# Optimization experiments

Hardware: AMD Instinct MI355X
Metric: run time of the kernel (lower is better)

The kernel has to match this reference:

```python
import jax, jax.numpy as jnp
import numpy as np
from jax import lax

RATE = 2
KSIZE = 3
FUSE_K = 3
PAD = 1
SCALE = 10.0
ESCAPE_NAN = 1e-4
DN = ('NCHW', 'OIHW', 'NCHW')


def _patches(x, k, s, p):
    # x: [C,H,W] -> [L, C, k, k]  (matches torch pad + unfold(2).unfold(3) + permute)
    C = x.shape[0]
    pt = lax.conv_general_dilated_patches(
        x[None], (k, k), (s, s), [(p, p), (p, p)], dimension_numbers=DN)[0]
    oh, ow = pt.shape[1], pt.shape[2]
    # feature dim ordered (c, kh, kw)
    return pt.reshape(C, k, k, oh * ow).transpose(3, 0, 1, 2)


def setup_inputs() -> dict:
    key = jax.random.key(0)
    k1, k2 = jax.random.split(key)
    f = jax.random.normal(k1, (2, 128, 128, 128), dtype=jnp.float32)
    b = jax.random.normal(k2, (2, 128, 128, 128), dtype=jnp.float32)
    mask = jnp.zeros((1, 1, 128, 128), dtype=jnp.float32)
    return {"f": f, "b": b, "mask": mask}


def reference(f, b, mask):
    B, C, H, W = f.shape
    kernel = 2 * RATE  # 4
    # raw background patches (values for conv_transpose), per sample: [L, C, 4, 4]
    raw_w = jax.vmap(lambda bi: _patches(bi, kernel, RATE, PAD))(b)
    # nearest downsample by rate (torch nearest with scale 1/2 == strided slice)
    fd = f[:, :, ::RATE, ::RATE]
    bd = b[:, :, ::RATE, ::RATE]
    md = mask[:, :, ::RATE, ::RATE]
    fh, fw = fd.shape[2], fd.shape[3]
    bh, bw = bd.shape[2], bd.shape[3]
    L = bh * bw
    # matching (key) patches: [B, L, C, 3, 3]
    w = jax.vmap(lambda bi: _patches(bi, KSIZE, 1, PAD))(bd)
    # mask patches -> mm[l] = 1 where patch mean == 0 (valid background)
    m = _patches(md[0], KSIZE, 1, PAD)           # [L, 1, 3, 3]
    mm = (jnp.mean(m, axis=(1, 2, 3)) == 0.0).astype(f.dtype)[:, None, None]  # [L,1,1]

    fuse_w = jnp.eye(FUSE_K, dtype=f.dtype).reshape(1, 1, FUSE_K, FUSE_K)

    def fuse_conv(y):
        return lax.conv_general_dilated(y, fuse_w, (1, 1), [(1, 1), (1, 1)],
                                        dimension_numbers=DN)

    def one(xi, wi, rwi):
        # xi: [C,fh,fw], wi: [L,C,3,3], rwi: [L,C,4,4]
        norm = jnp.sqrt(jnp.sum(wi * wi, axis=(1, 2, 3), keepdims=True))
        wn = wi / jnp.maximum(norm, ESCAPE_NAN)
        # correlation scores (QK^T analogue): [1, L, fh, fw]
        yi = lax.conv_general_dilated(xi[None], wn, (1, 1), [(1, 1), (1, 1)],
                                      dimension_numbers=DN)
        # diagonal fuse convs, exactly mirroring the torch view/permute sequence
        yi = yi.reshape(1, 1, fh * fw, bh * bw)
        yi = fuse_conv(yi)
        yi = yi.reshape(fh, fw, bh, bw).transpose(1, 0, 3, 2).reshape(1, 1, fh * fw, bh * bw)
        yi = fuse_conv(yi)
        yi = yi.reshape(fw, fh, bw, bh).transpose(1, 0, 3, 2)  # [fh, fw, bh, bw]
        # faithful to the torch .view (plain contiguous reshape, no transpose)
        yi = yi.reshape(bh * bw, fh, fw)
        yi = yi * mm
        yi = jax.nn.softmax(yi * SCALE, axis=0) * mm
        # conv_transpose2d(yi, rwi, stride=rate, padding=1) / 4
        wt = jnp.flip(rwi, axis=(2, 3)).transpose(1, 0, 2, 3)  # [C, L, 4, 4]
        p = kernel - 1 - PAD  # 2
        out = lax.conv_general_dilated(yi[None], wt, (1, 1), [(p, p), (p, p)],
                                       lhs_dilation=(RATE, RATE),
                                       dimension_numbers=DN) / 4.0
        return out[0]  # [C, H, W]

    y = jax.vmap(one)(fd, w, raw_w)  # [B, C, H, W]
    return y
```

## Files before the change

### kernel.cpp

```cpp
#include <hip/hip_runtime.h>

#define CC 128
#define HH 128
#define WW 128
#define DH 64
#define DW 64
#define LTOT 4096
#define K0S 384
#define K2 2048
#define SCALE_F 10.0f
#define IMG ((size_t)CC * HH * WW)

typedef __attribute__((ext_vector_type(8))) short short8;
typedef __attribute__((ext_vector_type(4))) float f32x4;

struct Prep4 { const float* src[4]; unsigned short* dst[4]; float* ssq[4]; int lo[4]; };
struct PtrN2 { const float* ssq[2]; float* invn[2]; float* mmv[2]; };
struct PtrR2 { const float* src[2]; unsigned short* dst[2]; };

__device__ __forceinline__ unsigned short f2bf(float x) {
    union { float f; unsigned u; } v; v.f = x;
    unsigned r = v.u + 0x7fffu + ((v.u >> 16) & 1u);
    return (unsigned short)(r >> 16);
}
__device__ __forceinline__ float bf2f(unsigned short b) {
    union { unsigned u; float f; } v; v.u = ((unsigned)b) << 16;
    return v.f;
}

#define GLDS16(g, l) __builtin_amdgcn_global_load_lds( \
    (const __attribute__((address_space(1))) void*)(g), \
    (__attribute__((address_space(3))) void*)(l), 16, 0, 0)

__global__ __launch_bounds__(128) void split_ds_kernel(Prep4 P) {
    __shared__ float partial[2];
    int z = blockIdx.z;
    const float* __restrict__ src = P.src[z];
    unsigned short* __restrict__ dst = P.dst[z];
    int lo_in_seg1 = P.lo[z];
    int n = blockIdx.x;
    int c = threadIdx.x;
    int ny = n >> 6, nx = n & 63;
    float v = src[((size_t)c * HH + 2 * ny) * WW + 2 * nx];
    unsigned short hi = f2bf(v);
    unsigned short lo = f2bf(v - bf2f(hi));
    unsigned short* drow = dst + (size_t)n * K0S;
    drow[c]       = hi;
    drow[128 + c] = lo_in_seg1 ? lo : hi;
    drow[256 + c] = lo_in_seg1 ? hi : lo;

    float* ssq = P.ssq[z];
    if (ssq) {
        float s2 = v * v;
#pragma unroll
        for (int o = 32; o; o >>= 1) s2 += __shfl_xor(s2, o);
        if ((threadIdx.x & 63) == 0) partial[threadIdx.x >> 6] = s2;
        __syncthreads();
        if (threadIdx.x == 0) ssq[n] = partial[0] + partial[1];
    }
}

__global__ __launch_bounds__(256) void im2col_rawt_kernel(PtrR2 P) {
    int z = blockIdx.z;
    const float* __restrict__ src = P.src[z];
    unsigned short* __restrict__ dst = P.dst[z];
    int idx = blockIdx.x * 256 + threadIdx.x;
    int p = idx & (LTOT - 1);
    int m = idx >> 12;
    int px = p & 63, py = p >> 6;
    int ke = m & 3, kd = (m >> 2) & 3, c = m >> 4;
    int yy = 2 * py - 1 + kd, xx = 2 * px - 1 + ke;
    float v = 0.f;
    if (yy >= 0 && yy < HH && xx >= 0 && xx < WW)
        v = src[((size_t)c * HH + yy) * WW + xx];
    dst[idx] = f2bf(v);
}

__global__ void norm_mm_kernel(PtrN2 P, const float* __restrict__ mask) {
    int z = blockIdx.z;
    const float* __restrict__ ssq = P.ssq[z];
    float* __restrict__ inv_norm = P.invn[z];
    float* __restrict__ mmv = P.mmv[z];
    int p = blockIdx.x * blockDim.x + threadIdx.x;
    int px = p & 63, py = p >> 6;
    float s = 0.f, ms = 0.f;
    for (int di = -1; di <= 1; ++di)
        for (int dj = -1; dj <= 1; ++dj) {
            int y = py + di, x = px + dj;
            if (y >= 0 && y < DH && x >= 0 && x < DW) {
                s += ssq[y * 64 + x];
                ms += mask[(size_t)(2 * y) * WW + 2 * x];
            }
        }
    float n = sqrtf(s);
    if (n < 1e-4f) n = 1e-4f;
    inv_norm[p] = 1.f / n;
    mmv[p] = (ms == 0.f) ? 1.f : 0.f;
}

__global__ __launch_bounds__(256) void gemm_mfma(
    const unsigned short* __restrict__ Aop, const unsigned short* __restrict__ Bop,
    float* __restrict__ C, int M, int N, int K)
{
    __shared__ short As[128 * 64];
    __shared__ short Bs[128 * 64];
    int tid = threadIdx.x;
    int wave = tid >> 6, lane = tid & 63;
    int wm = (wave >> 1) * 64;
    int wn = (wave & 1) * 64;
    int bm = blockIdx.y * 128, bn = blockIdx.x * 128;

    int rowS = wave * 32;
    int lrow8 = lane >> 3;
    int gchunk = ((lane & 7) ^ lrow8) * 8;

    f32x4 acc[4][4] = {};

    int quad = lane >> 4;
    int r16 = lane & 15;
    int pc0 = ((quad)     ^ (r16 & 7)) * 8;
    int pc1 = ((4 + quad) ^ (r16 & 7)) * 8;

    const unsigned short* ap0 = Aop + (size_t)(bm + rowS +  0 + lrow8) * K + gchunk;
    const unsigned short* ap1 = Aop + (size_t)(bm + rowS +  8 + lrow8) * K + gchunk;
    const unsigned short* ap2 = Aop + (size_t)(bm + rowS + 16 + lrow8) * K + gchunk;
    const unsigned short* ap3 = Aop + (size_t)(bm + rowS + 24 + lrow8) * K + gchunk;
    const unsigned short* bp0 = Bop + (size_t)(bn + rowS +  0 + lrow8) * K + gchunk;
    const unsigned short* bp1 = Bop + (size_t)(bn + rowS +  8 + lrow8) * K + gchunk;
    const unsigned short* bp2 = Bop + (size_t)(bn + rowS + 16 + lrow8) * K + gchunk;
    const unsigned short* bp3 = Bop + (size_t)(bn + rowS + 24 + lrow8) * K + gchunk;
    short* lA = As + rowS * 64;
    short* lB = Bs + rowS * 64;

    for (int k0 = 0; k0 < K; k0 += 64) {
        GLDS16(ap0, lA);            GLDS16(ap1, lA + 8 * 64);
        GLDS16(ap2, lA + 16 * 64);  GLDS16(ap3, lA + 24 * 64);
        GLDS16(bp0, lB);            GLDS16(bp1, lB + 8 * 64);
        GLDS16(bp2, lB + 16 * 64);  GLDS16(bp3, lB + 24 * 64);
        ap0 += 64; ap1 += 64; ap2 += 64; ap3 += 64;
        bp0 += 64; bp1 += 64; bp2 += 64; bp3 += 64;
        __syncthreads();

        short8 a0[4], b0[4], a1[4], b1[4];
#pragma unroll
        for (int i = 0; i < 4; ++i) {
            a0[i] = *(const short8*)&As[(wm + i * 16 + r16) * 64 + pc0];
            b0[i] = *(const short8*)&Bs[(wn + i * 16 + r16) * 64 + pc0];
            a1[i] = *(const short8*)&As[(wm + i * 16 + r16) * 64 + pc1];
            b1[i] = *(const short8*)&Bs[(wn + i * 16 + r16) * 64 + pc1];
        }
#pragma unroll
        for (int i = 0; i < 4; ++i)
#pragma unroll
            for (int j = 0; j < 4; ++j) {
                acc[i][j] = __builtin_amdgcn_mfma_f32_16x16x32_bf16(a0[i], b0[j], acc[i][j], 0, 0, 0);
                acc[i][j] = __builtin_amdgcn_mfma_f32_16x16x32_bf16(a1[i], b1[j], acc[i][j], 0, 0, 0);
            }
        __syncthreads();
    }

    int col = lane & 15, rq = (lane >> 4) * 4;
#pragma unroll
    for (int i = 0; i < 4; ++i) {
#pragma unroll
        for (int r = 0; r < 4; ++r) {
            int m = bm + wm + i * 16 + rq + r;
#pragma unroll
            for (int j = 0; j < 4; ++j)
                C[(size_t)m * N + bn + wn + j * 16 + col] = acc[i][j][r];
        }
    }
}

__global__ __launch_bounds__(256) void stencil_norm_kernel(
    const float* __restrict__ C, const float* __restrict__ invn,
    float* __restrict__ Sout)
{
    int blk = blockIdx.x;
    int q = ((blk & 7) << 9) | (blk >> 3);
    int t = threadIdx.x;
    int qy = q >> 6, qx = q & 63;
    int px = t & 63;
    int py0 = t >> 6;
    float acc[16] = {};
#pragma unroll
    for (int du = -1; du <= 1; ++du) {
        if (qy + du < 0 || qy + du > 63) continue;
#pragma unroll
        for (int dv = -1; dv <= 1; ++dv) {
            if (qx + dv < 0 || qx + dv > 63) continue;
            if (px + dv < 0 || px + dv > 63) continue;
            const float* row = C + (size_t)(q + 64 * du + dv) * LTOT + 64 * du + dv;
#pragma unroll
            for (int i = 0; i < 16; ++i) {
                int py = py0 + 4 * i;
                if (py + du < 0 || py + du > 63) continue;
                acc[i] += row[t + 256 * i];
            }
        }
    }
    float* orow = Sout + (size_t)q * LTOT;
#pragma unroll
    for (int i = 0; i < 16; ++i)
        orow[t + 256 * i] = acc[i] * invn[t + 256 * i];
}

__global__ __launch_bounds__(256, 4) void fused_conv_softmax_kernel(
    const float* __restrict__ S, const float* __restrict__ mmv,
    unsigned short* __restrict__ S16)
{
    __shared__ float redmax[4];
    __shared__ float redsum[4];
    int blk = blockIdx.x;
    int q = ((blk & 7) << 9) | (blk >> 3);
    int t = threadIdx.x;
    int lane = t & 63, wid = t >> 6;

    int rbase = ((q & 63) << 6) | (q >> 6);
    int rrs[3];
    bool rok[3];
#pragma unroll
    for (int j = 0; j < 3; ++j) {
        int r2 = rbase + (j - 1);
        rok[j] = (r2 >= 0) && (r2 < LTOT);
        rrs[j] = ((r2 & 63) << 6) | ((r2 >> 6) & 63);
    }

    float v[16], m[16];
#pragma unroll
    for (int i = 0; i < 16; ++i) {
        int c = t + (i << 8);
        int cbase = ((c & 63) << 6) | (c >> 6);
        float s = 0.f;
#pragma unroll
        for (int j = 0; j < 3; ++j) {
            if (!rok[j]) continue;
            int c2 = cbase + (j - 1);
            if (c2 < 0 || c2 >= LTOT) continue;
            int cc = ((c2 & 63) << 6) | (c2 >> 6);
            int rr = rrs[j];
            float tsum = 0.f;
#pragma unroll
            for (int d1 = -1; d1 <= 1; ++d1) {
                int a = rr + d1, bcol = cc + d1;
                if (a >= 0 && a < LTOT && bcol >= 0 && bcol < LTOT)
                    tsum += S[(size_t)a * LTOT + bcol];
            }
            s += tsum;
        }
        float mmx = mmv[c];
        m[i] = mmx;
        v[i] = s * mmx * SCALE_F;
    }

    float mx = v[0];
#pragma unroll
    for (int i = 1; i < 16; ++i) mx = fmaxf(mx, v[i]);
#pragma unroll
    for (int o = 32; o; o >>= 1) mx = fmaxf(mx, __shfl_xor(mx, o));
    if (lane == 0) redmax[wid] = mx;
    __syncthreads();
    float gmx = fmaxf(fmaxf(redmax[0], redmax[1]), fmaxf(redmax[2], redmax[3]));

    float s = 0.f;
#pragma unroll
    for (int i = 0; i < 16; ++i) {
        v[i] = __expf(v[i] - gmx);
        s += v[i];
    }
#pragma unroll
    for (int o = 32; o; o >>= 1) s += __shfl_xor(s, o);
    if (lane == 0) redsum[wid] = s;
    __syncthreads();
    float inv = 1.f / (redsum[0] + redsum[1] + redsum[2] + redsum[3]);

    unsigned short* orow = S16 + (size_t)q * LTOT;
#pragma unroll
    for (int i = 0; i < 16; ++i)
        orow[t + (i << 8)] = f2bf(v[i] * inv * m[i]);
}

__global__ void output_kernel(const float* __restrict__ C2t, float* __restrict__ out) {
    int idx = blockIdx.x * blockDim.x + threadIdx.x;
    int x = idx & 127;
    int y = (idx >> 7) & 127;
    int c = idx >> 14;
    int oylo = max(0, (y - 1) >> 1), oyhi = min(63, (y + 1) >> 1);
    int oxlo = max(0, (x - 1) >> 1), oxhi = min(63, (x + 1) >> 1);
    float s = 0.f;
    for (int oy = oylo; oy <= oyhi; ++oy)
        for (int ox = oxlo; ox <= oxhi; ++ox) {
            int kd = y - 2 * oy + 1;
            int ke = x - 2 * ox + 1;
            s += C2t[(size_t)(c * 16 + kd * 4 + ke) * LTOT + oy * 64 + ox];
        }
    out[idx] = s * 0.25f;
}

extern "C" void kernel_launch(void* const* d_in, const int* in_sizes, int n_in,
                              void* d_out, int out_size, void* d_ws, size_t ws_size,
                              hipStream_t stream) {
    (void)in_sizes; (void)n_in; (void)out_size; (void)ws_size;
    const float* f    = (const float*)d_in[0];
    const float* b    = (const float*)d_in[1];
    const float* mask = (const float*)d_in[2];
    float* out = (float*)d_out;

    const size_t SZ_MAT = (size_t)LTOT * LTOT * 4;
    const size_t SZ_WR  = (size_t)K2 * LTOT * 2;
    const size_t SZ_SP  = (size_t)LTOT * K0S * 2;
    const size_t SZ_V   = (size_t)LTOT * 4;

    auto pad = [](size_t n) { return (n + 255) & ~(size_t)255; };
    char* p = (char*)d_ws;
    auto take = [&](size_t n) -> void* { void* r = (void*)p; p += pad(n); return r; };

    float* Buf1 = (float*)take(SZ_MAT);
    float* Buf2 = (float*)take(SZ_MAT);
    unsigned short* W0 = (unsigned short*)take(SZ_WR);
    unsigned short* W1 = (unsigned short*)take(SZ_WR);
    unsigned short* Bsp0 = (unsigned short*)take(SZ_SP);
    unsigned short* Fsp0 = (unsigned short*)take(SZ_SP);
    unsigned short* Bsp1 = (unsigned short*)take(SZ_SP);
    unsigned short* Fsp1 = (unsigned short*)take(SZ_SP);
    float* ssq0 = (float*)take(SZ_V);  float* ssq1 = (float*)take(SZ_V);
    float* invn0 = (float*)take(SZ_V); float* invn1 = (float*)take(SZ_V);
    float* mmv0 = (float*)take(SZ_V);  float* mmv1 = (float*)take(SZ_V);

    const float* f0 = f,  *b0 = b;
    const float* f1 = f + IMG, *b1 = b + IMG;

    unsigned short* S16 = (unsigned short*)Buf1;
    float* C2t = Buf2;

    Prep4 P{{b0, f0, b1, f1}, {Bsp0, Fsp0, Bsp1, Fsp1},
            {ssq0, nullptr, ssq1, nullptr}, {1, 0, 1, 0}};
    split_ds_kernel<<<dim3(LTOT, 1, 4), 128, 0, stream>>>(P);
    PtrN2 nm{{ssq0, ssq1}, {invn0, invn1}, {mmv0, mmv1}};
    norm_mm_kernel<<<dim3(16, 1, 2), 256, 0, stream>>>(nm, mask);
    PtrR2 rw{{b0, b1}, {W0, W1}};
    im2col_rawt_kernel<<<dim3((size_t)K2 * LTOT / 256, 1, 2), 256, 0, stream>>>(rw);

    for (int bi = 0; bi < 2; ++bi) {
        const unsigned short* Fsp = bi ? Fsp1 : Fsp0;
        const unsigned short* Bsp = bi ? Bsp1 : Bsp0;
        const unsigned short* W   = bi ? W1 : W0;
        const float* invn = bi ? invn1 : invn0;
        const float* mmv  = bi ? mmv1 : mmv0;

        gemm_mfma<<<dim3(32, 32), 256, 0, stream>>>(Fsp, Bsp, Buf1, LTOT, LTOT, K0S);

        stencil_norm_kernel<<<LTOT, 256, 0, stream>>>(Buf1, invn, Buf2);

        fused_conv_softmax_kernel<<<LTOT, 256, 0, stream>>>(Buf2, mmv, S16);

        gemm_mfma<<<dim3(LTOT / 128, K2 / 128), 256, 0, stream>>>(W, S16, C2t, K2, LTOT, LTOT);

        output_kernel<<<CC * HH * WW / 256, 256, 0, stream>>>(C2t, out + (size_t)bi * IMG);
    }
}
```

Before: 598.7 us.

## Pad score matrix and vectorize stencil and fused softmax kernels

Writes the normalized score matrix into a zero-padded buffer with a row stride of 4104 floats, so the fused diagonal-conv/softmax kernel can read contiguous 16-float chunks with vector loads instead of bounds-checked scattered scalar loads. The stencil kernel now handles 16 contiguous columns per thread with vectorized loads and stores, and the softmax output is written as short8 vectors. The raw-patch im2col moves into the per-batch loop using one shared buffer, which reduces workspace. The trade-offs are unaligned vector loads, extra zeroing of the guard rows and columns, and a dependence on those zeroed pads being correct.

```diff
diff --git a/kernel.cpp b/kernel.cpp
--- a/kernel.cpp
+++ b/kernel.cpp
@@ -10,6 +10,7 @@
 #define K2 2048
 #define SCALE_F 10.0f
 #define IMG ((size_t)CC * HH * WW)
+#define PSTR 4104
 
 typedef __attribute__((ext_vector_type(8))) short short8;
 typedef __attribute__((ext_vector_type(4))) float f32x4;
@@ -26,6 +27,10 @@
 __device__ __forceinline__ float bf2f(unsigned short b) {
     union { unsigned u; float f; } v; v.u = ((unsigned)b) << 16;
     return v.f;
+}
+
+__device__ __forceinline__ f32x4 ld4u(const float* p) {
+    f32x4 r; __builtin_memcpy(&r, p, 16); return r;
 }
 
 #define GLDS16(g, l) __builtin_amdgcn_global_load_lds( \
@@ -174,39 +179,57 @@
 
 __global__ __launch_bounds__(256) void stencil_norm_kernel(
     const float* __restrict__ C, const float* __restrict__ invn,
-    float* __restrict__ Sout)
+    float* __restrict__ Sg)
 {
     int blk = blockIdx.x;
     int q = ((blk & 7) << 9) | (blk >> 3);
     int t = threadIdx.x;
     int qy = q >> 6, qx = q & 63;
-    int px = t & 63;
-    int py0 = t >> 6;
-    float acc[16] = {};
+    int chunk = t >> 2;
+    int lanebase = (t & 3) << 4;
+    int p0 = t << 4;
+
+    f32x4 acc[4];
+#pragma unroll
+    for (int g = 0; g < 4; ++g) { acc[g][0] = acc[g][1] = acc[g][2] = acc[g][3] = 0.f; }
+
 #pragma unroll
     for (int du = -1; du <= 1; ++du) {
         if (qy + du < 0 || qy + du > 63) continue;
+        if (chunk + du < 0 || chunk + du > 63) continue;
 #pragma unroll
         for (int dv = -1; dv <= 1; ++dv) {
             if (qx + dv < 0 || qx + dv > 63) continue;
-            if (px + dv < 0 || px + dv > 63) continue;
-            const float* row = C + (size_t)(q + 64 * du + dv) * LTOT + 64 * du + dv;
-#pragma unroll
-            for (int i = 0; i < 16; ++i) {
-                int py = py0 + 4 * i;
-                if (py + du < 0 || py + du > 63) continue;
-                acc[i] += row[t + 256 * i];
+            const float* rowp = C + (size_t)(q + 64 * du + dv) * LTOT + 64 * du + dv + p0;
+#pragma unroll
+            for (int g = 0; g < 4; ++g) {
+                f32x4 lv = ld4u(rowp + 4 * g);
+                if (dv == -1 && g == 0 && lanebase == 0)  lv[0] = 0.f;
+                if (dv ==  1 && g == 3 && lanebase == 48) lv[3] = 0.f;
+                acc[g] += lv;
             }
         }
     }
-    float* orow = Sout + (size_t)q * LTOT;
-#pragma unroll
-    for (int i = 0; i < 16; ++i)
-        orow[t + 256 * i] = acc[i] * invn[t + 256 * i];
-}
-
-__global__ __launch_bounds__(256, 4) void fused_conv_softmax_kernel(
-    const float* __restrict__ S, const float* __restrict__ mmv,
+    float* orow = Sg + (size_t)q * PSTR;
+#pragma unroll
+    for (int g = 0; g < 4; ++g) {
+        f32x4 iv = *(const f32x4*)(invn + p0 + 4 * g);
+        *(f32x4*)(orow + p0 + 4 * g) = acc[g] * iv;
+    }
+    if (t == 0) { orow[-4] = orow[-3] = orow[-2] = orow[-1] = 0.f; }
+    else if (t == 1) { orow[4096] = orow[4097] = orow[4098] = orow[4099] = 0.f; }
+    if (q == 0) {
+        float* gr = Sg - 4 - PSTR;
+        for (int k = t; k < PSTR; k += 256) gr[k] = 0.f;
+    }
+    if (q == 4095) {
+        float* gr = Sg - 4 + (size_t)4096 * PSTR;
+        for (int k = t; k < PSTR; k += 256) gr[k] = 0.f;
+    }
+}
+
+__global__ __launch_bounds__(256) void fused_conv_softmax_kernel(
+    const float* __restrict__ Sg, const float* __restrict__ mmv,
     unsigned short* __restrict__ S16)
 {
     __shared__ float redmax[4];
@@ -215,43 +238,50 @@
     int q = ((blk & 7) << 9) | (blk >> 3);
     int t = threadIdx.x;
     int lane = t & 63, wid = t >> 6;
+    int chunk = t >> 2;
+    int lanebase = (t & 3) << 4;
+    int c0 = t << 4;
 
     int rbase = ((q & 63) << 6) | (q >> 6);
-    int rrs[3];
-    bool rok[3];
+
+    f32x4 sacc[4];
+#pragma unroll
+    for (int g = 0; g < 4; ++g) { sacc[g][0] = sacc[g][1] = sacc[g][2] = sacc[g][3] = 0.f; }
+
 #pragma unroll
     for (int j = 0; j < 3; ++j) {
         int r2 = rbase + (j - 1);
-        rok[j] = (r2 >= 0) && (r2 < LTOT);
-        rrs[j] = ((r2 & 63) << 6) | ((r2 >> 6) & 63);
-    }
-
-    float v[16], m[16];
-#pragma unroll
-    for (int i = 0; i < 16; ++i) {
-        int c = t + (i << 8);
-        int cbase = ((c & 63) << 6) | (c >> 6);
-        float s = 0.f;
-#pragma unroll
-        for (int j = 0; j < 3; ++j) {
-            if (!rok[j]) continue;
-            int c2 = cbase + (j - 1);
-            if (c2 < 0 || c2 >= LTOT) continue;
-            int cc = ((c2 & 63) << 6) | (c2 >> 6);
-            int rr = rrs[j];
-            float tsum = 0.f;
-#pragma unroll
-            for (int d1 = -1; d1 <= 1; ++d1) {
-                int a = rr + d1, bcol = cc + d1;
-                if (a >= 0 && a < LTOT && bcol >= 0 && bcol < LTOT)
-                    tsum += S[(size_t)a * LTOT + bcol];
-            }
-            s += tsum;
-        }
-        float mmx = mmv[c];
-        m[i] = mmx;
-        v[i] = s * mmx * SCALE_F;
-    }
+        if (r2 < 0 || r2 >= LTOT) continue;
+        int rr = ((r2 & 63) << 6) | (r2 >> 6);
+        int cj = chunk + (j - 1);
+        int ccb;
+        if (cj < 0)       ccb = 4031 + lanebase;
+        else if (cj > 63) ccb = lanebase + 1;
+        else              ccb = (cj << 6) + lanebase;
+        const float* pr = Sg + (size_t)rr * PSTR + ccb;
+#pragma unroll
+        for (int g = 0; g < 4; ++g) {
+            const float* pg = pr + 4 * g;
+            f32x4 lm = ld4u(pg - (PSTR + 1));
+            f32x4 l0 = ld4u(pg);
+            f32x4 lp = ld4u(pg + (PSTR + 1));
+            f32x4 tj = lm + l0 + lp;
+            if (j == 0 && g == 0 && t == 0)   tj[0] = 0.f;
+            if (j == 2 && g == 3 && t == 255) tj[3] = 0.f;
+            sacc[g] += tj;
+        }
+    }
+
+    float v[16];
+#pragma unroll
+    for (int g = 0; g < 4; ++g) {
+        f32x4 m4 = *(const f32x4*)(mmv + c0 + 4 * g);
+#pragma unroll
+        for (int e = 0; e < 4; ++e)
+            v[4 * g + e] = sacc[g][e] * m4[e] * SCALE_F;
+    }
+#pragma unroll
+    for (int k = 0; k < 16; ++k) asm volatile("" : "+v"(v[k]));
 
     float mx = v[0];
 #pragma unroll
@@ -274,10 +304,15 @@
     __syncthreads();
     float inv = 1.f / (redsum[0] + redsum[1] + redsum[2] + redsum[3]);
 
-    unsigned short* orow = S16 + (size_t)q * LTOT;
-#pragma unroll
-    for (int i = 0; i < 16; ++i)
-        orow[t + (i << 8)] = f2bf(v[i] * inv * m[i]);
+    unsigned short* orow = S16 + (size_t)q * LTOT + c0;
+    short8 h0, h1;
+#pragma unroll
+    for (int e = 0; e < 8; ++e) {
+        h0[e] = (short)f2bf(v[e]     * inv * mmv[c0 + e]);
+        h1[e] = (short)f2bf(v[8 + e] * inv * mmv[c0 + 8 + e]);
+    }
+    *(short8*)orow = h0;
+    *(short8*)(orow + 8) = h1;
 }
 
 __global__ void output_kernel(const float* __restrict__ C2t, float* __restrict__ out) {
@@ -306,19 +341,20 @@
     const float* mask = (const float*)d_in[2];
     float* out = (float*)d_out;
 
-    const size_t SZ_MAT = (size_t)LTOT * LTOT * 4;
-    const size_t SZ_WR  = (size_t)K2 * LTOT * 2;
-    const size_t SZ_SP  = (size_t)LTOT * K0S * 2;
-    const size_t SZ_V   = (size_t)LTOT * 4;
+    const size_t SZ_MAT  = (size_t)LTOT * LTOT * 4;
+    const size_t SZ_SPAD = (size_t)PSTR * 4098 * 4;
+    const size_t SZ_WR   = (size_t)K2 * LTOT * 2;
+    const size_t SZ_SP   = (size_t)LTOT * K0S * 2;
+    const size_t SZ_V    = (size_t)LTOT * 4;
 
     auto pad = [](size_t n) { return (n + 255) & ~(size_t)255; };
     char* p = (char*)d_ws;
     auto take = [&](size_t n) -> void* { void* r = (void*)p; p += pad(n); return r; };
 
+    take(256);
     float* Buf1 = (float*)take(SZ_MAT);
-    float* Buf2 = (float*)take(SZ_MAT);
-    unsigned short* W0 = (unsigned short*)take(SZ_WR);
-    unsigned short* W1 = (unsigned short*)take(SZ_WR);
+    float* Spad = (float*)take(SZ_SPAD);
+    unsigned short* W = (unsigned short*)take(SZ_WR);
     unsigned short* Bsp0 = (unsigned short*)take(SZ_SP);
     unsigned short* Fsp0 = (unsigned short*)take(SZ_SP);
     unsigned short* Bsp1 = (unsigned short*)take(SZ_SP);
@@ -330,29 +366,30 @@
     const float* f0 = f,  *b0 = b;
     const float* f1 = f + IMG, *b1 = b + IMG;
 
+    float* Sg = Spad + PSTR + 4;
     unsigned short* S16 = (unsigned short*)Buf1;
-    float* C2t = Buf2;
+    float* C2t = Spad;
 
     Prep4 P{{b0, f0, b1, f1}, {Bsp0, Fsp0, Bsp1, Fsp1},
             {ssq0, nullptr, ssq1, nullptr}, {1, 0, 1, 0}};
     split_ds_kernel<<<dim3(LTOT, 1, 4), 128, 0, stream>>>(P);
     PtrN2 nm{{ssq0, ssq1}, {invn0, invn1}, {mmv0, mmv1}};
     norm_mm_kernel<<<dim3(16, 1, 2), 256, 0, stream>>>(nm, mask);
-    PtrR2 rw{{b0, b1}, {W0, W1}};
-    im2col_rawt_kernel<<<dim3((size_t)K2 * LTOT / 256, 1, 2), 256, 0, stream>>>(rw);
 
     for (int bi = 0; bi < 2; ++bi) {
         const unsigned short* Fsp = bi ? Fsp1 : Fsp0;
         const unsigned short* Bsp = bi ? Bsp1 : Bsp0;
-        const unsigned short* W   = bi ? W1 : W0;
         const float* invn = bi ? invn1 : invn0;
         const float* mmv  = bi ? mmv1 : mmv0;
 
+        PtrR2 rw{{bi ? b1 : b0, nullptr}, {W, nullptr}};
+        im2col_rawt_kernel<<<dim3((size_t)K2 * LTOT / 256, 1, 1), 256, 0, stream>>>(rw);
+
         gemm_mfma<<<dim3(32, 32), 256, 0, stream>>>(Fsp, Bsp, Buf1, LTOT, LTOT, K0S);
 
-        stencil_norm_kernel<<<LTOT, 256, 0, stream>>>(Buf1, invn, Buf2);
-
-        fused_conv_softmax_kernel<<<LTOT, 256, 0, stream>>>(Buf2, mmv, S16);
+        stencil_norm_kernel<<<LTOT, 256, 0, stream>>>(Buf1, invn, Sg);
+
+        fused_conv_softmax_kernel<<<LTOT, 256, 0, stream>>>(Sg, mmv, S16);
 
         gemm_mfma<<<dim3(LTOT / 128, K2 / 128), 256, 0, stream>>>(W, S16, C2t, K2, LTOT, LTOT);
 
```

Measured after the change: 547.3 us. -8.6%, faster.
